# Optimization experiments

Hardware: AMD Instinct MI355X
Metric: run time of the kernel (lower is better)

The kernel has to match this reference:

```python
import jax, jax.numpy as jnp
import numpy as np

IN_FEATURES = 4096
OUT_FEATURES = 16384
BATCH = 2
SEQ = 2048


def setup_inputs() -> dict:
    key = jax.random.key(0)
    k_x, k_s, k_sgn, k_b = jax.random.split(key, 4)
    x = jax.random.normal(k_x, (BATCH, SEQ, IN_FEATURES), dtype=jnp.float32)
    # stored: uint8-style inverse-log magnitudes in [1, 255]
    stored = jax.random.randint(k_s, (OUT_FEATURES, IN_FEATURES), 1, 256, dtype=jnp.int32)
    # sign in {0,1}; mapped to {-1,+1} inside reference
    sign = jax.random.randint(k_sgn, (OUT_FEATURES, IN_FEATURES), 0, 2, dtype=jnp.int32)
    # log range matching typical weight magnitudes exp(-8)..exp(0)
    log_min = jnp.full((1,), -8.0, dtype=jnp.float32)
    log_max = jnp.full((1,), 0.0, dtype=jnp.float32)
    bias = jax.random.normal(k_b, (OUT_FEATURES,), dtype=jnp.float32) * 0.02
    return {"x": x, "stored": stored, "sign": sign, "log_min": log_min,
            "log_max": log_max, "bias": bias}


def _dequant_qins(stored, sign, log_min, log_max):
    # reverse inverse mapping: stored in [1,255] -> normalized in [0,1]
    normalized = (255.0 - stored.astype(jnp.float32)) / 254.0
    log_weight = log_min + normalized * (log_max - log_min)
    sign_f = (2 * sign - 1).astype(jnp.float32)  # {0,1} -> {-1,+1}
    return sign_f * jnp.exp(log_weight)  # [out, in] fp32


def reference(x, stored, sign, log_min, log_max, bias):
    lmin = log_min[0]
    lmax = log_max[0]
    w = _dequant_qins(stored, sign, lmin, lmax)  # [O, I]
    # F.linear: y = x @ w.T + bias
    out = jnp.einsum('bsi,oi->bso', x, w) + bias
    return out
```

## Files before the change

kernel.cpp:

```cpp
#include <hip/hip_runtime.h>
#include <stdint.h>

#define M_DIM 4096
#define N_DIM 16384
#define K_DIM 4096
#define BM 256
#define BN 256
#define BK 64
#define NT (K_DIM / BK)

typedef __attribute__((ext_vector_type(8))) __bf16 bf16x8;
typedef __attribute__((ext_vector_type(4))) float f32x4;

__device__ __forceinline__ unsigned short f2bf(float f) {
    uint32_t u = __builtin_bit_cast(uint32_t, f);
    uint32_t r = (u + 0x7FFFu + ((u >> 16) & 1u)) >> 16;
    return (unsigned short)r;
}

union Pack8 { unsigned short h[8]; uint4 v; };

__device__ __forceinline__ void async_copy16(const void* g, void* l) {
    __builtin_amdgcn_global_load_lds((__attribute__((address_space(1))) void*)(g),
                                     (__attribute__((address_space(3))) void*)(l),
                                     16, 0, 0);
}

#define BARRIER() do { asm volatile("" ::: "memory"); \
                       __builtin_amdgcn_s_barrier();  \
                       asm volatile("" ::: "memory"); } while (0)

__global__ __launch_bounds__(256) void cast_x_kernel(const float* __restrict__ x,
                                                     unsigned short* __restrict__ xb,
                                                     int n8) {
    for (int i = blockIdx.x * blockDim.x + threadIdx.x; i < n8;
         i += gridDim.x * blockDim.x) {
        const float4* p = (const float4*)(x + (size_t)i * 8);
        float4 v0 = p[0], v1 = p[1];
        Pack8 o;
        o.h[0] = f2bf(v0.x); o.h[1] = f2bf(v0.y);
        o.h[2] = f2bf(v0.z); o.h[3] = f2bf(v0.w);
        o.h[4] = f2bf(v1.x); o.h[5] = f2bf(v1.y);
        o.h[6] = f2bf(v1.z); o.h[7] = f2bf(v1.w);
        *(uint4*)(xb + (size_t)i * 8) = o.v;
    }
}

__global__ __launch_bounds__(256) void dequant_kernel(const int* __restrict__ stored,
                                                      const int* __restrict__ sign,
                                                      const float* __restrict__ log_min,
                                                      const float* __restrict__ log_max,
                                                      unsigned short* __restrict__ wb,
                                                      int n8) {
    const float lmin = log_min[0];
    const float lrange = log_max[0] - lmin;
    for (int i = blockIdx.x * blockDim.x + threadIdx.x; i < n8;
         i += gridDim.x * blockDim.x) {
        const int4* ps = (const int4*)(stored + (size_t)i * 8);
        const int4* pg = (const int4*)(sign + (size_t)i * 8);
        int4 s0 = ps[0], s1 = ps[1];
        int4 g0 = pg[0], g1 = pg[1];
        int sv[8] = {s0.x, s0.y, s0.z, s0.w, s1.x, s1.y, s1.z, s1.w};
        int gv[8] = {g0.x, g0.y, g0.z, g0.w, g1.x, g1.y, g1.z, g1.w};
        Pack8 o;
#pragma unroll
        for (int j = 0; j < 8; ++j) {
            float nrm = (255.0f - (float)sv[j]) * (1.0f / 254.0f);
            float w = __expf(lmin + nrm * lrange);
            o.h[j] = f2bf(gv[j] ? w : -w);
        }
        *(uint4*)(wb + (size_t)i * 8) = o.v;
    }
}

__global__ __launch_bounds__(512, 2) void gemm_kernel(const unsigned short* __restrict__ A,
                                                      const unsigned short* __restrict__ W,
                                                      const float* __restrict__ bias,
                                                      float* __restrict__ C) {
    extern __shared__ char lds[];
    const int tid  = threadIdx.x;
    const int wave = tid >> 6;
    const int lane = tid & 63;
    const int l15  = lane & 15;
    const int l16  = lane >> 4;
    const int wr   = wave >> 2;
    const int wc   = wave & 3;

    const int bid = blockIdx.x;
    const int wg  = ((bid & 7) << 7) | (bid >> 3);
    const int rowBase = (wg >> 6) * BM;
    const int colBase = (wg & 63) * BN;

    f32x4 acc[8][4] = {};

    auto stage_half = [&](int t, int u) {
        const int kb = t * BK;
        const unsigned short* g = (u < 2) ? A : W;
        const int rb = ((u < 2) ? rowBase : colBase) + (u & 1) * 128;
        char* hb = lds + ((u < 2) ? (t % 3) * 32768
                                  : 98304 + (t & 1) * 32768) + (u & 1) * 16384;
#pragma unroll
        for (int sub = 0; sub < 2; ++sub) {
            const int Ld   = (sub * 512 + tid) * 16;
            const int r    = Ld >> 7;
            const int colb = (Ld & 127) ^ ((r & 7) << 4);
            async_copy16(g + (size_t)(rb + r) * K_DIM + kb + (colb >> 1),
                         hb + (sub * 512 + wave * 64) * 16);
        }
    };

    stage_half(0, 0); stage_half(0, 1);
    stage_half(0, 2); stage_half(0, 3);
    stage_half(1, 0); stage_half(1, 1);

    for (int t = 0; t < NT; ++t) {
        if (t + 1 < NT) asm volatile("s_waitcnt vmcnt(4)" ::: "memory");
        else            asm volatile("s_waitcnt vmcnt(0)" ::: "memory");
        BARRIER();
        __builtin_amdgcn_sched_barrier(0);

        if (t + 1 < NT) { stage_half(t + 1, 2); stage_half(t + 1, 3); }
        if (t + 2 < NT) { stage_half(t + 2, 0); stage_half(t + 2, 1); }

        const char* bA  = lds + (t % 3) * 32768 + wr * 16384;
        const char* bB  = lds + 98304 + (t & 1) * 32768 + (wc >> 1) * 16384;
        const int   brB = (wc & 1) * 64;

        bf16x8 aF0[4][2], aF1[4][2], bF0[2][2], bF1[2][2];

#pragma unroll
        for (int i = 0; i < 4; ++i)
#pragma unroll
            for (int ks = 0; ks < 2; ++ks) {
                const int r    = i * 16 + l15;
                const int colb = (ks * 64 + l16 * 16) ^ ((r & 7) << 4);
                aF0[i][ks] = *(const bf16x8*)(bA + (r << 7) + colb);
            }
#pragma unroll
        for (int j = 0; j < 2; ++j)
#pragma unroll
            for (int ks = 0; ks < 2; ++ks) {
                const int r    = brB + j * 16 + l15;
                const int colb = (ks * 64 + l16 * 16) ^ ((r & 7) << 4);
                bF0[j][ks] = *(const bf16x8*)(bB + (r << 7) + colb);
            }
#pragma unroll
        for (int j = 0; j < 2; ++j)
#pragma unroll
            for (int ks = 0; ks < 2; ++ks) {
                const int r    = brB + 32 + j * 16 + l15;
                const int colb = (ks * 64 + l16 * 16) ^ ((r & 7) << 4);
                bF1[j][ks] = *(const bf16x8*)(bB + (r << 7) + colb);
            }
        __builtin_amdgcn_s_setprio(1);
#pragma unroll
        for (int i = 0; i < 4; ++i)
#pragma unroll
            for (int j = 0; j < 2; ++j)
#pragma unroll
                for (int ks = 0; ks < 2; ++ks)
                    acc[i][j] = __builtin_amdgcn_mfma_f32_16x16x32_bf16(
                        aF0[i][ks], bF0[j][ks], acc[i][j], 0, 0, 0);
        __builtin_amdgcn_s_setprio(0);

#pragma unroll
        for (int i = 0; i < 4; ++i)
#pragma unroll
            for (int ks = 0; ks < 2; ++ks) {
                const int r    = 64 + i * 16 + l15;
                const int colb = (ks * 64 + l16 * 16) ^ ((r & 7) << 4);
                aF1[i][ks] = *(const bf16x8*)(bA + (r << 7) + colb);
            }
        __builtin_amdgcn_s_setprio(1);
#pragma unroll
        for (int i = 0; i < 4; ++i)
#pragma unroll
            for (int j = 0; j < 2; ++j)
#pragma unroll
                for (int ks = 0; ks < 2; ++ks)
                    acc[i][2 + j] = __builtin_amdgcn_mfma_f32_16x16x32_bf16(
                        aF0[i][ks], bF1[j][ks], acc[i][2 + j], 0, 0, 0);
        __builtin_amdgcn_s_setprio(0);

        __builtin_amdgcn_s_setprio(1);
#pragma unroll
        for (int i = 0; i < 4; ++i)
#pragma unroll
            for (int j = 0; j < 2; ++j)
#pragma unroll
                for (int ks = 0; ks < 2; ++ks)
                    acc[4 + i][j] = __builtin_amdgcn_mfma_f32_16x16x32_bf16(
                        aF1[i][ks], bF0[j][ks], acc[4 + i][j], 0, 0, 0);
        __builtin_amdgcn_s_setprio(0);

        __builtin_amdgcn_s_setprio(1);
#pragma unroll
        for (int i = 0; i < 4; ++i)
#pragma unroll
            for (int j = 0; j < 2; ++j)
#pragma unroll
                for (int ks = 0; ks < 2; ++ks)
                    acc[4 + i][2 + j] = __builtin_amdgcn_mfma_f32_16x16x32_bf16(
                        aF1[i][ks], bF1[j][ks], acc[4 + i][2 + j], 0, 0, 0);
        __builtin_amdgcn_s_setprio(0);
    }

#pragma unroll
    for (int m = 0; m < 8; ++m) {
        const int grow0 = rowBase + wr * 128 + m * 16 + l16 * 4;
#pragma unroll
        for (int n = 0; n < 4; ++n) {
            const int gcol = colBase + wc * 64 + n * 16 + l15;
            const float bv = bias[gcol];
#pragma unroll
            for (int r4 = 0; r4 < 4; ++r4)
                C[(size_t)(grow0 + r4) * N_DIM + gcol] = acc[m][n][r4] + bv;
        }
    }
}

extern "C" void kernel_launch(void* const* d_in, const int* in_sizes, int n_in,
                              void* d_out, int out_size, void* d_ws, size_t ws_size,
                              hipStream_t stream) {
    const float* x       = (const float*)d_in[0];
    const int*   stored  = (const int*)d_in[1];
    const int*   sign    = (const int*)d_in[2];
    const float* log_min = (const float*)d_in[3];
    const float* log_max = (const float*)d_in[4];
    const float* bias    = (const float*)d_in[5];
    float* out = (float*)d_out;

    unsigned short* Ab = (unsigned short*)d_ws;
    unsigned short* Wb = (unsigned short*)((char*)d_ws +
                          (size_t)M_DIM * K_DIM * sizeof(unsigned short));

    cast_x_kernel<<<2048, 256, 0, stream>>>(x, Ab, (M_DIM * K_DIM) / 8);
    dequant_kernel<<<4096, 256, 0, stream>>>(stored, sign, log_min, log_max, Wb,
                                             (N_DIM * K_DIM) / 8);

    hipFuncSetAttribute((const void*)gemm_kernel,
                        hipFuncAttributeMaxDynamicSharedMemorySize, 163840);
    gemm_kernel<<<dim3((M_DIM / BM) * (N_DIM / BN)), dim3(512), 163840, stream>>>(
        Ab, Wb, bias, out);
}
```

Before: 612.2 us.

## Software-pipeline LDS fragment loads across K iterations with rotating buffers

Restructures the main GEMM loop so the barrier and next-tile prefetch sit mid-iteration, after three of the four MFMA quadrants. The first fragments of the next K tile are then loaded from LDS while the last quadrant's MFMAs run. Buffers rotate via pointer swaps, and A is staged three tiles ahead and B two. The aim is to hide LDS read latency and the barrier stall behind matrix math. The cost is more live fragment registers, trickier vmcnt accounting, and a risk of races if the wait counts are off.

```diff
diff --git a/kernel.cpp b/kernel.cpp
--- a/kernel.cpp
+++ b/kernel.cpp
@@ -93,106 +93,134 @@
 
     f32x4 acc[8][4] = {};
 
-    auto stage_half = [&](int t, int u) {
+    auto stage_tile = [&](const unsigned short* g, int rb0, int t, char* buf) {
         const int kb = t * BK;
-        const unsigned short* g = (u < 2) ? A : W;
-        const int rb = ((u < 2) ? rowBase : colBase) + (u & 1) * 128;
-        char* hb = lds + ((u < 2) ? (t % 3) * 32768
-                                  : 98304 + (t & 1) * 32768) + (u & 1) * 16384;
-#pragma unroll
-        for (int sub = 0; sub < 2; ++sub) {
-            const int Ld   = (sub * 512 + tid) * 16;
-            const int r    = Ld >> 7;
-            const int colb = (Ld & 127) ^ ((r & 7) << 4);
-            async_copy16(g + (size_t)(rb + r) * K_DIM + kb + (colb >> 1),
-                         hb + (sub * 512 + wave * 64) * 16);
+#pragma unroll
+        for (int h = 0; h < 2; ++h) {
+            char* hb = buf + h * 16384;
+            const int rb = rb0 + h * 128;
+#pragma unroll
+            for (int sub = 0; sub < 2; ++sub) {
+                const int Ld   = (sub * 512 + tid) * 16;
+                const int r    = Ld >> 7;
+                const int colb = (Ld & 127) ^ ((r & 7) << 4);
+                async_copy16(g + (size_t)(rb + r) * K_DIM + kb + (colb >> 1),
+                             hb + (sub * 512 + wave * 64) * 16);
+            }
         }
     };
 
-    stage_half(0, 0); stage_half(0, 1);
-    stage_half(0, 2); stage_half(0, 3);
-    stage_half(1, 0); stage_half(1, 1);
+    char* pA0 = lds;
+    char* pA1 = lds + 32768;
+    char* pA2 = lds + 65536;
+    char* pB0 = lds + 98304;
+    char* pB1 = lds + 131072;
+
+    stage_tile(A, rowBase, 0, pA0);
+    stage_tile(W, colBase, 0, pB0);
+    stage_tile(A, rowBase, 1, pA1);
+    stage_tile(W, colBase, 1, pB1);
+    stage_tile(A, rowBase, 2, pA2);
+    asm volatile("s_waitcnt vmcnt(12)" ::: "memory");
+    BARRIER();
+
+    const int bAoff = wr * 16384;
+    const int bBoff = (wc >> 1) * 16384;
+    const int brB   = (wc & 1) * 64;
+
+    bf16x8 aF0[4][2], aF1[4][2], bF0[2][2], bF1[2][2];
+
+#pragma unroll
+    for (int i = 0; i < 4; ++i)
+#pragma unroll
+        for (int ks = 0; ks < 2; ++ks) {
+            const int r    = i * 16 + l15;
+            const int colb = (ks * 64 + l16 * 16) ^ ((r & 7) << 4);
+            aF0[i][ks] = *(const bf16x8*)(pA0 + bAoff + (r << 7) + colb);
+        }
+#pragma unroll
+    for (int j = 0; j < 2; ++j)
+#pragma unroll
+        for (int ks = 0; ks < 2; ++ks) {
+            const int r    = brB + j * 16 + l15;
+            const int colb = (ks * 64 + l16 * 16) ^ ((r & 7) << 4);
+            bF0[j][ks] = *(const bf16x8*)(pB0 + bBoff + (r << 7) + colb);
+        }
 
     for (int t = 0; t < NT; ++t) {
-        if (t + 1 < NT) asm volatile("s_waitcnt vmcnt(4)" ::: "memory");
+#pragma unroll
+        for (int i = 0; i < 4; ++i)
+#pragma unroll
+            for (int ks = 0; ks < 2; ++ks) {
+                const int r    = 64 + i * 16 + l15;
+                const int colb = (ks * 64 + l16 * 16) ^ ((r & 7) << 4);
+                aF1[i][ks] = *(const bf16x8*)(pA0 + bAoff + (r << 7) + colb);
+            }
+#pragma unroll
+        for (int j = 0; j < 2; ++j)
+#pragma unroll
+            for (int ks = 0; ks < 2; ++ks) {
+                const int r    = brB + 32 + j * 16 + l15;
+                const int colb = (ks * 64 + l16 * 16) ^ ((r & 7) << 4);
+                bF1[j][ks] = *(const bf16x8*)(pB0 + bBoff + (r << 7) + colb);
+            }
+        __builtin_amdgcn_s_setprio(1);
+#pragma unroll
+        for (int i = 0; i < 4; ++i)
+#pragma unroll
+            for (int j = 0; j < 2; ++j)
+#pragma unroll
+                for (int ks = 0; ks < 2; ++ks)
+                    acc[i][j] = __builtin_amdgcn_mfma_f32_16x16x32_bf16(
+                        aF0[i][ks], bF0[j][ks], acc[i][j], 0, 0, 0);
+        __builtin_amdgcn_s_setprio(0);
+
+        __builtin_amdgcn_s_setprio(1);
+#pragma unroll
+        for (int i = 0; i < 4; ++i)
+#pragma unroll
+            for (int j = 0; j < 2; ++j)
+#pragma unroll
+                for (int ks = 0; ks < 2; ++ks)
+                    acc[i][2 + j] = __builtin_amdgcn_mfma_f32_16x16x32_bf16(
+                        aF0[i][ks], bF1[j][ks], acc[i][2 + j], 0, 0, 0);
+        __builtin_amdgcn_s_setprio(0);
+
+        __builtin_amdgcn_s_setprio(1);
+#pragma unroll
+        for (int i = 0; i < 4; ++i)
+#pragma unroll
+            for (int j = 0; j < 2; ++j)
+#pragma unroll
+                for (int ks = 0; ks < 2; ++ks)
+                    acc[4 + i][j] = __builtin_amdgcn_mfma_f32_16x16x32_bf16(
+                        aF1[i][ks], bF0[j][ks], acc[4 + i][j], 0, 0, 0);
+        __builtin_amdgcn_s_setprio(0);
+        if (t + 2 < NT) asm volatile("s_waitcnt vmcnt(4)" ::: "memory");
         else            asm volatile("s_waitcnt vmcnt(0)" ::: "memory");
         BARRIER();
         __builtin_amdgcn_sched_barrier(0);
 
-        if (t + 1 < NT) { stage_half(t + 1, 2); stage_half(t + 1, 3); }
-        if (t + 2 < NT) { stage_half(t + 2, 0); stage_half(t + 2, 1); }
-
-        const char* bA  = lds + (t % 3) * 32768 + wr * 16384;
-        const char* bB  = lds + 98304 + (t & 1) * 32768 + (wc >> 1) * 16384;
-        const int   brB = (wc & 1) * 64;
-
-        bf16x8 aF0[4][2], aF1[4][2], bF0[2][2], bF1[2][2];
-
-#pragma unroll
-        for (int i = 0; i < 4; ++i)
-#pragma unroll
-            for (int ks = 0; ks < 2; ++ks) {
-                const int r    = i * 16 + l15;
-                const int colb = (ks * 64 + l16 * 16) ^ ((r & 7) << 4);
-                aF0[i][ks] = *(const bf16x8*)(bA + (r << 7) + colb);
-            }
-#pragma unroll
-        for (int j = 0; j < 2; ++j)
-#pragma unroll
-            for (int ks = 0; ks < 2; ++ks) {
-                const int r    = brB + j * 16 + l15;
-                const int colb = (ks * 64 + l16 * 16) ^ ((r & 7) << 4);
-                bF0[j][ks] = *(const bf16x8*)(bB + (r << 7) + colb);
-            }
-#pragma unroll
-        for (int j = 0; j < 2; ++j)
-#pragma unroll
-            for (int ks = 0; ks < 2; ++ks) {
-                const int r    = brB + 32 + j * 16 + l15;
-                const int colb = (ks * 64 + l16 * 16) ^ ((r & 7) << 4);
-                bF1[j][ks] = *(const bf16x8*)(bB + (r << 7) + colb);
-            }
-        __builtin_amdgcn_s_setprio(1);
-#pragma unroll
-        for (int i = 0; i < 4; ++i)
-#pragma unroll
-            for (int j = 0; j < 2; ++j)
-#pragma unroll
-                for (int ks = 0; ks < 2; ++ks)
-                    acc[i][j] = __builtin_amdgcn_mfma_f32_16x16x32_bf16(
-                        aF0[i][ks], bF0[j][ks], acc[i][j], 0, 0, 0);
-        __builtin_amdgcn_s_setprio(0);
-
-#pragma unroll
-        for (int i = 0; i < 4; ++i)
-#pragma unroll
-            for (int ks = 0; ks < 2; ++ks) {
-                const int r    = 64 + i * 16 + l15;
-                const int colb = (ks * 64 + l16 * 16) ^ ((r & 7) << 4);
-                aF1[i][ks] = *(const bf16x8*)(bA + (r << 7) + colb);
-            }
-        __builtin_amdgcn_s_setprio(1);
-#pragma unroll
-        for (int i = 0; i < 4; ++i)
-#pragma unroll
-            for (int j = 0; j < 2; ++j)
-#pragma unroll
-                for (int ks = 0; ks < 2; ++ks)
-                    acc[i][2 + j] = __builtin_amdgcn_mfma_f32_16x16x32_bf16(
-                        aF0[i][ks], bF1[j][ks], acc[i][2 + j], 0, 0, 0);
-        __builtin_amdgcn_s_setprio(0);
-
-        __builtin_amdgcn_s_setprio(1);
-#pragma unroll
-        for (int i = 0; i < 4; ++i)
-#pragma unroll
-            for (int j = 0; j < 2; ++j)
-#pragma unroll
-                for (int ks = 0; ks < 2; ++ks)
-                    acc[4 + i][j] = __builtin_amdgcn_mfma_f32_16x16x32_bf16(
-                        aF1[i][ks], bF0[j][ks], acc[4 + i][j], 0, 0, 0);
-        __builtin_amdgcn_s_setprio(0);
-
+        if (t + 2 < NT) stage_tile(W, colBase, t + 2, pB0);
+        if (t + 3 < NT) stage_tile(A, rowBase, t + 3, pA0);
+        if (t + 1 < NT) {
+#pragma unroll
+            for (int i = 0; i < 4; ++i)
+#pragma unroll
+                for (int ks = 0; ks < 2; ++ks) {
+                    const int r    = i * 16 + l15;
+                    const int colb = (ks * 64 + l16 * 16) ^ ((r & 7) << 4);
+                    aF0[i][ks] = *(const bf16x8*)(pA1 + bAoff + (r << 7) + colb);
+                }
+#pragma unroll
+            for (int j = 0; j < 2; ++j)
+#pragma unroll
+                for (int ks = 0; ks < 2; ++ks) {
+                    const int r    = brB + j * 16 + l15;
+                    const int colb = (ks * 64 + l16 * 16) ^ ((r & 7) << 4);
+                    bF0[j][ks] = *(const bf16x8*)(pB1 + bBoff + (r << 7) + colb);
+                }
+        }
         __builtin_amdgcn_s_setprio(1);
 #pragma unroll
         for (int i = 0; i < 4; ++i)
@@ -203,6 +231,9 @@
                     acc[4 + i][2 + j] = __builtin_amdgcn_mfma_f32_16x16x32_bf16(
                         aF1[i][ks], bF1[j][ks], acc[4 + i][2 + j], 0, 0, 0);
         __builtin_amdgcn_s_setprio(0);
+
+        char* ta = pA0; pA0 = pA1; pA1 = pA2; pA2 = ta;
+        char* tb = pB0; pB0 = pB1; pB1 = tb;
     }
 
 #pragma unroll
```

New measurement: 618.9 us. Within noise of the previous version (+1.1%).
